# Optimization experiments

Hardware: AMD Instinct MI355X
Metric: run time of the kernel (lower is better)

Reference implementation:

```python
import jax, jax.numpy as jnp
import numpy as np

EPS = 1e-6

def rms_norm(x):
    # x / sqrt(mean(x^2, axis=-1) + eps)
    return x * jax.lax.rsqrt(jnp.mean(x * x, axis=-1, keepdims=True) + EPS)

def setup_inputs() -> dict:
    key = jax.random.key(0)
    k1, k2, k3 = jax.random.split(key, 3)
    T, B, D = 2048, 16, 1024
    x = jax.random.normal(k1, (T, B, D), dtype=jnp.float32)
    h0 = jax.random.normal(k2, (B, D), dtype=jnp.float32)
    # Orthogonal-ish init scaled by 0.5 (faithful to nn.init.orthogonal_ then *0.5)
    A = jax.random.normal(k3, (D, D), dtype=jnp.float32)
    Q, _ = jnp.linalg.qr(A)
    W = 0.5 * Q
    b = jnp.zeros((D,), dtype=jnp.float32)
    log_alpha = jnp.asarray(np.log(0.1), dtype=jnp.float32)
    return {"x": x, "h0": h0, "W": W, "b": b, "log_alpha": log_alpha}

def reference(x, h0, W, b, log_alpha):
    T, B, D = x.shape
    alpha = jnp.exp(log_alpha)
    # Precompute Wx for all timesteps: [T, B, D]
    Wx_all = jnp.einsum('tbd,ed->tbe', x, W) + b

    def step(h_prev, wx_t):
        h_raw = h_prev + alpha * wx_t
        h_new = rms_norm(h_raw)
        out = h_new * jax.nn.silu(h_new)
        return h_new, (h_new, out)

    _, (h_seq, output) = jax.lax.scan(step, h0, Wx_all)
    h = jnp.concatenate([h0[None], h_seq], axis=0)  # [T+1, B, D]
    return output, h
```

## Files before the change

### kernel.cpp

```cpp
#include <hip/hip_runtime.h>
#include <hip/hip_bf16.h>

#define TT 2048
#define BB 16
#define DD 1024
#define BD (BB*DD)
#define MR (TT*BB)
#define EPSV 1e-6f
#define INVD (1.0f/1024.0f)
#define CH 256
#define NCH (TT/CH)
#define RING 8

typedef __bf16 bf16x8_t __attribute__((ext_vector_type(8)));
typedef float  f32x4_t  __attribute__((ext_vector_type(4)));
typedef float  f32x2    __attribute__((ext_vector_type(2)));
typedef __attribute__((address_space(1))) void gvoid_t;
typedef __attribute__((address_space(3))) void lvoid_t;
typedef __attribute__((address_space(3))) float2 lds_f2;

union F4 { f32x4_t q; float4 v; f32x2 h[2]; float f[4]; };

static __device__ __forceinline__ f32x2 pk_mul(f32x2 a, f32x2 b) {
    f32x2 d; asm("v_pk_mul_f32 %0, %1, %2" : "=v"(d) : "v"(a), "v"(b)); return d;
}
static __device__ __forceinline__ f32x2 pk_fma(f32x2 a, f32x2 b, f32x2 c) {
    f32x2 d; asm("v_pk_fma_f32 %0, %1, %2, %3" : "=v"(d) : "v"(a), "v"(b), "v"(c)); return d;
}
static __device__ __forceinline__ f32x2 pk_add(f32x2 a, f32x2 b) {
    f32x2 d; asm("v_pk_add_f32 %0, %1, %2" : "=v"(d) : "v"(a), "v"(b)); return d;
}
static __device__ __forceinline__ float wave_red_sum(float ss) {
    asm volatile(
        "s_nop 1\n\t"
        "v_add_f32 %0, %0, %0 row_shr:1 bound_ctrl:0\n\t"
        "s_nop 1\n\t"
        "v_add_f32 %0, %0, %0 row_shr:2 bound_ctrl:0\n\t"
        "s_nop 1\n\t"
        "v_add_f32 %0, %0, %0 row_shr:4 bank_mask:0xe\n\t"
        "s_nop 1\n\t"
        "v_add_f32 %0, %0, %0 row_shr:8 bank_mask:0xc\n\t"
        "s_nop 1\n\t"
        "v_add_f32 %0, %0, %0 row_bcast:15 row_mask:0xa\n\t"
        "s_nop 1\n\t"
        "v_add_f32 %0, %0, %0 row_bcast:31 row_mask:0xc\n\t"
        "s_nop 1"
        : "+v"(ss));
    return __builtin_bit_cast(float, __builtin_amdgcn_readlane(__builtin_bit_cast(int, ss), 63));
}

static __device__ __forceinline__ unsigned short f2bf(float f) {
    __hip_bfloat16 h = __float2bfloat16(f);
    return __builtin_bit_cast(unsigned short, h);
}

__global__ void k_convert(const float* __restrict__ x, const float* __restrict__ W,
                          unsigned short* __restrict__ xb, unsigned short* __restrict__ wb) {
    const long NX4 = (long)MR * DD / 4;
    const long NW4 = (long)DD * DD / 4;
    const long stride = (long)gridDim.x * blockDim.x;
    for (long j = (long)blockIdx.x * blockDim.x + threadIdx.x; j < NX4 + NW4; j += stride) {
        const float4* src; unsigned short* dst; long o;
        if (j < NX4) { src = (const float4*)x; dst = xb; o = j; }
        else         { src = (const float4*)W; dst = wb; o = j - NX4; }
        float4 v = src[o];
        ushort4 u;
        u.x = f2bf(v.x); u.y = f2bf(v.y); u.z = f2bf(v.z); u.w = f2bf(v.w);
        *(ushort4*)(dst + o * 4) = u;
    }
}

__global__ __launch_bounds__(256, 2)
void k_gemm(const unsigned short* __restrict__ A, const unsigned short* __restrict__ Bw,
            const float* __restrict__ bias, float* __restrict__ C) {
    __shared__ char lds[16384];
    char* ldsA = lds;
    char* ldsB = lds + 8192;
    const int tid  = threadIdx.x;
    const int lane = tid & 63;
    const int wid  = tid >> 6;
    const int wm = wid >> 1, wn = wid & 1;
    const size_t arow0 = (size_t)blockIdx.y * 128;
    const int    brow0 = blockIdx.x * 128;

    f32x4_t acc[4][4] = {};

    const int off0 = tid * 16,        row0_ = off0 >> 6, colb0 = off0 & 63;
    const int off1 = 4096 + tid * 16, row1_ = off1 >> 6, colb1 = off1 & 63;

    for (int kk = 0; kk < DD / 32; ++kk) {
        const int kbase = kk * 32;
        __builtin_amdgcn_global_load_lds(
            (gvoid_t*)(A + (arow0 + row0_) * DD + kbase + (colb0 >> 1)),
            (lvoid_t*)(ldsA + off0), 16, 0, 0);
        __builtin_amdgcn_global_load_lds(
            (gvoid_t*)(A + (arow0 + row1_) * DD + kbase + (colb1 >> 1)),
            (lvoid_t*)(ldsA + off1), 16, 0, 0);
        __builtin_amdgcn_global_load_lds(
            (gvoid_t*)(Bw + (size_t)(brow0 + row0_) * DD + kbase + (colb0 >> 1)),
            (lvoid_t*)(ldsB + off0), 16, 0, 0);
        __builtin_amdgcn_global_load_lds(
            (gvoid_t*)(Bw + (size_t)(brow0 + row1_) * DD + kbase + (colb1 >> 1)),
            (lvoid_t*)(ldsB + off1), 16, 0, 0);
        __syncthreads();

        const int ml = lane & 15;
        const int kh = (lane >> 4) * 16;
        bf16x8_t av[4], bv[4];
        #pragma unroll
        for (int i = 0; i < 4; ++i) {
            av[i] = *(const bf16x8_t*)(ldsA + (wm * 64 + i * 16 + ml) * 64 + kh);
            bv[i] = *(const bf16x8_t*)(ldsB + (wn * 64 + i * 16 + ml) * 64 + kh);
        }
        #pragma unroll
        for (int i = 0; i < 4; ++i)
            #pragma unroll
            for (int j = 0; j < 4; ++j)
                acc[i][j] = __builtin_amdgcn_mfma_f32_16x16x32_bf16(av[i], bv[j], acc[i][j], 0, 0, 0);
        __syncthreads();
    }

    const int rq = (lane >> 4) * 4;
    const int cl = lane & 15;
    #pragma unroll
    for (int i = 0; i < 4; ++i) {
        #pragma unroll
        for (int j = 0; j < 4; ++j) {
            const int n = brow0 + wn * 64 + j * 16 + cl;
            const float bb = bias[n];
            #pragma unroll
            for (int q = 0; q < 4; ++q) {
                const size_t m = arow0 + wm * 64 + i * 16 + rq + q;
                C[m * DD + n] = acc[i][j][q] + bb;
            }
        }
    }
}

__global__ __launch_bounds__(256)
void k_gq(const float* __restrict__ Wx, const float* __restrict__ la,
          float2* __restrict__ gq_g) {
    const int b = blockIdx.y;
    const int wid = threadIdx.x >> 6, lane = threadIdx.x & 63;
    const int j0 = blockIdx.x * 16 + wid * 4;
    const float alpha = expf(la[0]);
    const float a2 = alpha * alpha;
    const int dof = lane * 4;
    const float* base = Wx + b * DD + dof;

    F4 R[5][4];
    #pragma unroll
    for (int jj = 0; jj < 5; ++jj) {
        const int row = max(j0 - 1 + jj, 0);
        #pragma unroll
        for (int k = 0; k < 4; ++k)
            R[jj][k].v = *(const float4*)(base + (size_t)row * BD + k * 256);
    }
    float red[8];
    #pragma unroll
    for (int sI = 0; sI < 4; ++sI) {
        float g = 0.f, q = 0.f;
        #pragma unroll
        for (int k = 0; k < 4; ++k)
            #pragma unroll
            for (int j = 0; j < 4; ++j) {
                const float w0 = R[sI][k].f[j], w1 = R[sI + 1][k].f[j];
                g = fmaf(w0, w1, g);
                q = fmaf(w1, w1, q);
            }
        red[sI] = g; red[4 + sI] = q;
    }
    #pragma unroll
    for (int m = 1; m < 64; m <<= 1)
        #pragma unroll
        for (int k = 0; k < 8; ++k)
            red[k] += __shfl_xor(red[k], m, 64);
    if (lane == 0) {
        #pragma unroll
        for (int sI = 0; sI < 4; ++sI) {
            const int j = j0 + sI;
            gq_g[(size_t)b * TT + j] =
                make_float2(j == 0 ? 0.f : a2 * red[sI], a2 * red[4 + sI]);
        }
    }
}

__global__ __launch_bounds__(64, 1)
void k_phaseA(const float* __restrict__ Wx, const float* __restrict__ h0,
              const float* __restrict__ la, const float2* __restrict__ gq_g,
              float* __restrict__ hout, float* __restrict__ rtab) {
    __shared__ float2 gqlds[TT];
    const int b = blockIdx.x;
    const int lane = threadIdx.x;
    const int dof = lane * 4;
    const float alpha = expf(la[0]);
    const float* wbase = Wx + b * DD + dof;

    {
        const float4* src = (const float4*)(gq_g + (size_t)b * TT);
        float4* dst = (float4*)gqlds;
        #pragma unroll
        for (int i = 0; i < 16; ++i) dst[i * 64 + lane] = src[i * 64 + lane];
    }
    f32x2 hraw[8];
    #pragma unroll
    for (int k = 0; k < 4; ++k) {
        F4 u; u.v = *(const float4*)(h0 + b * DD + k * 256 + dof);
        hraw[2*k] = u.h[0]; hraw[2*k+1] = u.h[1];
        *(float4*)(hout + b * DD + k * 256 + dof) = u.v;
    }
    asm volatile("" :: "v"(hraw[0]), "v"(hraw[1]), "v"(hraw[2]), "v"(hraw[3]),
                       "v"(hraw[4]), "v"(hraw[5]), "v"(hraw[6]), "v"(hraw[7]));
    asm volatile("s_waitcnt lgkmcnt(0)" ::: "memory");
    __builtin_amdgcn_sched_barrier(0);

    F4 buf[RING][4];
    #pragma unroll
    for (int s = 0; s < RING; ++s) {
        const float* wp = wbase + (size_t)s * BD;
        #pragma unroll
        for (int k = 0; k < 4; ++k)
            asm volatile("global_load_dwordx4 %0, %1, off"
                         : "=v"(buf[s][k].q) : "v"(wp + k * 256));
    }
    asm volatile("s_waitcnt vmcnt(24)" ::: "memory");
    __builtin_amdgcn_sched_barrier(0);

    float ss, ee[2], vr1 = 1.f, vr2 = 1.f;
    {
        f32x2 sa = pk_mul(hraw[0], hraw[0]);
        #pragma unroll
        for (int p = 1; p < 8; ++p) sa = pk_fma(hraw[p], hraw[p], sa);
        ss = wave_red_sum(sa[0] + sa[1]);
        f32x2 da = pk_mul(hraw[0], buf[0][0].h[0]);
        f32x2 ea = pk_mul(hraw[0], buf[1][0].h[0]);
        #pragma unroll
        for (int p = 1; p < 8; ++p) {
            da = pk_fma(hraw[p], buf[0][p>>1].h[p&1], da);
            ea = pk_fma(hraw[p], buf[1][p>>1].h[p&1], ea);
        }
        ee[1] = alpha * wave_red_sum(da[0] + da[1]);
        ee[0] = alpha * wave_red_sum(ea[0] + ea[1]);
    }
    f32x2 g2v[2];
    asm volatile("ds_read_b64 %0, %1" : "=v"(g2v[1]) : "v"((lds_f2*)&gqlds[0]));
    asm volatile("ds_read_b64 %0, %1" : "=v"(g2v[0]) : "v"((lds_f2*)&gqlds[1]));
    asm volatile("s_waitcnt lgkmcnt(0)" ::: "memory");
    __builtin_amdgcn_sched_barrier(0);

    float r_keep = 0.f;

    for (int tt = 0; tt < TT; tt += RING) {
        #pragma unroll
        for (int s = 0; s < RING; ++s) {
            const int m = tt + s;
            const int pe = (s + 1) & 1;

            if (s == 0 && (tt & 255) == 0) {
                float* hp = hout + (size_t)tt * BD + b * DD;
                const f32x2 rr0 = {vr1, vr1};
                #pragma unroll
                for (int k = 0; k < 4; ++k) {
                    F4 u;
                    u.h[0] = pk_mul(rr0, hraw[2*k]);
                    u.h[1] = pk_mul(rr0, hraw[2*k+1]);
                    *(float4*)(hp + k * 256 + dof) = u.v;
                }
            }

            asm volatile("s_waitcnt vmcnt(20)" ::: "memory");
            __builtin_amdgcn_sched_barrier(0);
            asm volatile("s_waitcnt lgkmcnt(1)" ::: "memory");
            __builtin_amdgcn_sched_barrier(0);

            const float Dp = fmaf(vr2, ee[pe], g2v[pe][0]);
            const float u1 = fmaf(vr1, ss, Dp + Dp);
            ss = fmaf(vr1, u1, g2v[pe][1]);
            const float rt = __builtin_amdgcn_rsqf(fmaf(ss, INVD, EPSV));
            r_keep = (lane == (m & 63)) ? rt : r_keep;

            const f32x2 rr1 = {vr1, vr1};
            const f32x2 aav = {alpha, alpha};
            #pragma unroll
            for (int k = 0; k < 4; ++k) {
                hraw[2*k]   = pk_fma(rr1, hraw[2*k],   pk_mul(aav, buf[s][k].h[0]));
                hraw[2*k+1] = pk_fma(rr1, hraw[2*k+1], pk_mul(aav, buf[s][k].h[1]));
            }

            {
                const F4* B = buf[(s + 2) & (RING - 1)];
                f32x2 ea0 = pk_mul(hraw[0], B[0].h[0]);
                f32x2 ea1 = pk_mul(hraw[1], B[0].h[1]);
                f32x2 ea2 = pk_mul(hraw[2], B[1].h[0]);
                f32x2 ea3 = pk_mul(hraw[3], B[1].h[1]);
                ea0 = pk_fma(hraw[4], B[2].h[0], ea0);
                ea1 = pk_fma(hraw[5], B[2].h[1], ea1);
                ea2 = pk_fma(hraw[6], B[3].h[0], ea2);
                ea3 = pk_fma(hraw[7], B[3].h[1], ea3);
                ea0 = pk_add(ea0, ea1); ea2 = pk_add(ea2, ea3); ea0 = pk_add(ea0, ea2);
                ee[pe] = alpha * wave_red_sum(ea0[0] + ea0[1]);
            }

            asm volatile("ds_read_b64 %0, %1"
                         : "=v"(g2v[pe]) : "v"((lds_f2*)&gqlds[(m + 2) & (TT - 1)]));

            {
                const float* wp = wbase + (size_t)((m + RING) & (TT - 1)) * BD;
                #pragma unroll
                for (int k = 0; k < 4; ++k)
                    asm volatile("global_load_dwordx4 %0, %1, off"
                                 : "=v"(buf[s][k].q) : "v"(wp + k * 256));
            }

            vr2 = vr1; vr1 = rt;
        }

        if ((tt & 63) == 56)
            rtab[(size_t)b * TT + (tt - 56) + lane] = r_keep;
    }

    asm volatile("s_waitcnt vmcnt(0) lgkmcnt(0)" ::: "memory");
}

__global__ __launch_bounds__(256)
void k_phaseB(float* __restrict__ WxOut, float* __restrict__ hout,
              const float* __restrict__ rtab, const float* __restrict__ la) {
    const int col = blockIdx.x * 256 + threadIdx.x;
    const int c = blockIdx.y;
    const int b = col >> 10;
    const float alpha = expf(la[0]);
    const float* rr = rtab + b * TT;
    float h = hout[(size_t)(c * CH) * BD + col];
    const int t0 = c * CH + 1;
    float w = WxOut[(size_t)(t0 - 1) * BD + col];
    for (int s = 0; s < CH; ++s) {
        const int t = t0 + s;
        float wnext = 0.f;
        if (s + 1 < CH) wnext = WxOut[(size_t)t * BD + col];
        const float r = rr[t - 1];
        const float hraw = fmaf(alpha, w, h);
        const float hn = r * hraw;
        const float sg = 1.0f / (1.0f + __expf(-hn));
        WxOut[(size_t)(t - 1) * BD + col] = hn * hn * sg;
        if ((t & (CH - 1)) != 0 || t == TT)
            hout[(size_t)t * BD + col] = hn;
        h = hn;
        w = wnext;
    }
}

extern "C" void kernel_launch(void* const* d_in, const int* in_sizes, int n_in,
                              void* d_out, int out_size, void* d_ws, size_t ws_size,
                              hipStream_t stream) {
    (void)in_sizes; (void)n_in; (void)out_size; (void)ws_size;
    const float* x    = (const float*)d_in[0];
    const float* h0   = (const float*)d_in[1];
    const float* W    = (const float*)d_in[2];
    const float* bias = (const float*)d_in[3];
    const float* la   = (const float*)d_in[4];

    float* outr = (float*)d_out;
    float* hreg = outr + (size_t)TT * BD;
    unsigned short* xb = (unsigned short*)hreg;
    unsigned short* wb = xb + (size_t)MR * DD;
    float2* gq_g = (float2*)(hreg + BD);
    float*  rtab = (float*)d_ws;

    k_convert<<<2048, 256, 0, stream>>>(x, W, xb, wb);
    k_gemm<<<dim3(DD / 128, MR / 128), 256, 0, stream>>>(xb, wb, bias, outr);
    k_gq<<<dim3(TT / 16, BB), 256, 0, stream>>>(outr, la, gq_g);
    k_phaseA<<<BB, 64, 0, stream>>>(outr, h0, la, gq_g, hreg, rtab);
    k_phaseB<<<dim3(BD / 256, NCH), 256, 0, stream>>>(outr, hreg, rtab, la);
}
```

Measured before the change: 542.5 us.

## Stage Wx rows through an LDS ring filled by dedicated producer waves

The sequential recurrence kernel now launches 5 waves per batch row. Four producer waves stream Wx rows into a 32-row LDS ring via global_load_lds, and the single compute wave reads rows from LDS with ds_read_b128 instead of issuing its own global loads. The aim is to take global-memory latency off the serial critical path by prefetching deeper. The cost is a block-wide barrier every 8 timesteps, 128KB of LDS per block, and LDS read latency on each step in place of the register ring.

Measured after the change: 547.7 us. About the same (+1.0%).

```diff
diff --git a/kernel.cpp b/kernel.cpp
--- a/kernel.cpp
+++ b/kernel.cpp
@@ -10,13 +10,13 @@
 #define INVD (1.0f/1024.0f)
 #define CH 256
 #define NCH (TT/CH)
-#define RING 8
 
 typedef __bf16 bf16x8_t __attribute__((ext_vector_type(8)));
 typedef float  f32x4_t  __attribute__((ext_vector_type(4)));
 typedef float  f32x2    __attribute__((ext_vector_type(2)));
 typedef __attribute__((address_space(1))) void gvoid_t;
 typedef __attribute__((address_space(3))) void lvoid_t;
+typedef __attribute__((address_space(3))) float  lds_f;
 typedef __attribute__((address_space(3))) float2 lds_f2;
 
 union F4 { f32x4_t q; float4 v; f32x2 h[2]; float f[4]; };
@@ -185,22 +185,61 @@
     }
 }
 
-__global__ __launch_bounds__(64, 1)
+__global__ __launch_bounds__(320, 1)
 void k_phaseA(const float* __restrict__ Wx, const float* __restrict__ h0,
               const float* __restrict__ la, const float2* __restrict__ gq_g,
               float* __restrict__ hout, float* __restrict__ rtab) {
+    __shared__ float  ring[32 * DD];
     __shared__ float2 gqlds[TT];
     const int b = blockIdx.x;
-    const int lane = threadIdx.x;
+    const int tid = threadIdx.x;
+    const int wid = tid >> 6;
+    const int lane = tid & 63;
+    const float alpha = expf(la[0]);
+
+    if (wid > 0) {
+        const int l = wid - 1;
+        const float* src = Wx + b * DD + lane * 4;
+        #pragma unroll
+        for (int q = 0; q < 3; ++q)
+            #pragma unroll
+            for (int j = 0; j < 2; ++j) {
+                const int row = q * 8 + l * 2 + j;
+                #pragma unroll
+                for (int k = 0; k < 4; ++k)
+                    __builtin_amdgcn_global_load_lds(
+                        (gvoid_t*)(src + (size_t)row * BD + k * 256),
+                        (lvoid_t*)(ring + (row & 31) * DD + k * 256), 16, 0, 0);
+            }
+        asm volatile("s_waitcnt vmcnt(8)" ::: "memory");
+        __builtin_amdgcn_s_barrier();
+        for (int p = 0; p < 256; ++p) {
+            if (p <= 252) {
+                const int q = p + 3;
+                #pragma unroll
+                for (int j = 0; j < 2; ++j) {
+                    const int row = q * 8 + l * 2 + j;
+                    #pragma unroll
+                    for (int k = 0; k < 4; ++k)
+                        __builtin_amdgcn_global_load_lds(
+                            (gvoid_t*)(src + (size_t)row * BD + k * 256),
+                            (lvoid_t*)(ring + (row & 31) * DD + k * 256), 16, 0, 0);
+                }
+                asm volatile("s_waitcnt vmcnt(8)" ::: "memory");
+            } else {
+                asm volatile("s_waitcnt vmcnt(0)" ::: "memory");
+            }
+            __builtin_amdgcn_s_barrier();
+        }
+        return;
+    }
+
     const int dof = lane * 4;
-    const float alpha = expf(la[0]);
-    const float* wbase = Wx + b * DD + dof;
-
     {
-        const float4* src = (const float4*)(gq_g + (size_t)b * TT);
+        const float4* src4 = (const float4*)(gq_g + (size_t)b * TT);
         float4* dst = (float4*)gqlds;
         #pragma unroll
-        for (int i = 0; i < 16; ++i) dst[i * 64 + lane] = src[i * 64 + lane];
+        for (int i = 0; i < 16; ++i) dst[i * 64 + lane] = src4[i * 64 + lane];
     }
     f32x2 hraw[8];
     #pragma unroll
@@ -213,51 +252,48 @@
                        "v"(hraw[4]), "v"(hraw[5]), "v"(hraw[6]), "v"(hraw[7]));
     asm volatile("s_waitcnt lgkmcnt(0)" ::: "memory");
     __builtin_amdgcn_sched_barrier(0);
-
-    F4 buf[RING][4];
-    #pragma unroll
-    for (int s = 0; s < RING; ++s) {
-        const float* wp = wbase + (size_t)s * BD;
+    __builtin_amdgcn_s_barrier();
+
+    F4 wReg[4][4];
+    #pragma unroll
+    for (int j = 0; j < 4; ++j)
         #pragma unroll
         for (int k = 0; k < 4; ++k)
-            asm volatile("global_load_dwordx4 %0, %1, off"
-                         : "=v"(buf[s][k].q) : "v"(wp + k * 256));
-    }
-    asm volatile("s_waitcnt vmcnt(24)" ::: "memory");
-    __builtin_amdgcn_sched_barrier(0);
-
-    float ss, ee[2], vr1 = 1.f, vr2 = 1.f;
-    {
-        f32x2 sa = pk_mul(hraw[0], hraw[0]);
-        #pragma unroll
-        for (int p = 1; p < 8; ++p) sa = pk_fma(hraw[p], hraw[p], sa);
-        ss = wave_red_sum(sa[0] + sa[1]);
-        f32x2 da = pk_mul(hraw[0], buf[0][0].h[0]);
-        f32x2 ea = pk_mul(hraw[0], buf[1][0].h[0]);
-        #pragma unroll
-        for (int p = 1; p < 8; ++p) {
-            da = pk_fma(hraw[p], buf[0][p>>1].h[p&1], da);
-            ea = pk_fma(hraw[p], buf[1][p>>1].h[p&1], ea);
-        }
-        ee[1] = alpha * wave_red_sum(da[0] + da[1]);
-        ee[0] = alpha * wave_red_sum(ea[0] + ea[1]);
-    }
+            asm volatile("ds_read_b128 %0, %1"
+                         : "=v"(wReg[j][k].q)
+                         : "v"((lds_f*)(ring + j * DD + k * 256 + dof)));
     f32x2 g2v[2];
     asm volatile("ds_read_b64 %0, %1" : "=v"(g2v[1]) : "v"((lds_f2*)&gqlds[0]));
     asm volatile("ds_read_b64 %0, %1" : "=v"(g2v[0]) : "v"((lds_f2*)&gqlds[1]));
     asm volatile("s_waitcnt lgkmcnt(0)" ::: "memory");
     __builtin_amdgcn_sched_barrier(0);
 
+    float ss, ee[2], vr1 = 1.f, vr2 = 1.f;
+    {
+        f32x2 sa = pk_mul(hraw[0], hraw[0]);
+        #pragma unroll
+        for (int p = 1; p < 8; ++p) sa = pk_fma(hraw[p], hraw[p], sa);
+        ss = wave_red_sum(sa[0] + sa[1]);
+        f32x2 da = pk_mul(hraw[0], wReg[0][0].h[0]);
+        f32x2 ea = pk_mul(hraw[0], wReg[1][0].h[0]);
+        #pragma unroll
+        for (int p = 1; p < 8; ++p) {
+            da = pk_fma(hraw[p], wReg[0][p>>1].h[p&1], da);
+            ea = pk_fma(hraw[p], wReg[1][p>>1].h[p&1], ea);
+        }
+        ee[1] = alpha * wave_red_sum(da[0] + da[1]);
+        ee[0] = alpha * wave_red_sum(ea[0] + ea[1]);
+    }
     float r_keep = 0.f;
 
-    for (int tt = 0; tt < TT; tt += RING) {
-        #pragma unroll
-        for (int s = 0; s < RING; ++s) {
-            const int m = tt + s;
+    for (int p = 0; p < 256; ++p) {
+        #pragma unroll
+        for (int s = 0; s < 8; ++s) {
+            const int m = p * 8 + s;
             const int pe = (s + 1) & 1;
 
-            if (s == 0 && (tt & 255) == 0) {
-                float* hp = hout + (size_t)tt * BD + b * DD;
+            if (s == 0 && (p & 31) == 0) {
+                float* hp = hout + (size_t)m * BD + b * DD;
                 const f32x2 rr0 = {vr1, vr1};
                 #pragma unroll
                 for (int k = 0; k < 4; ++k) {
@@ -268,9 +304,7 @@
                 }
             }
 
-            asm volatile("s_waitcnt vmcnt(20)" ::: "memory");
-            __builtin_amdgcn_sched_barrier(0);
-            asm volatile("s_waitcnt lgkmcnt(1)" ::: "memory");
+            asm volatile("s_waitcnt lgkmcnt(5)" ::: "memory");
             __builtin_amdgcn_sched_barrier(0);
 
             const float Dp = fmaf(vr2, ee[pe], g2v[pe][0]);
@@ -283,12 +317,12 @@
             const f32x2 aav = {alpha, alpha};
             #pragma unroll
             for (int k = 0; k < 4; ++k) {
-                hraw[2*k]   = pk_fma(rr1, hraw[2*k],   pk_mul(aav, buf[s][k].h[0]));
-                hraw[2*k+1] = pk_fma(rr1, hraw[2*k+1], pk_mul(aav, buf[s][k].h[1]));
+                hraw[2*k]   = pk_fma(rr1, hraw[2*k],   pk_mul(aav, wReg[s & 3][k].h[0]));
+                hraw[2*k+1] = pk_fma(rr1, hraw[2*k+1], pk_mul(aav, wReg[s & 3][k].h[1]));
             }
 
             {
-                const F4* B = buf[(s + 2) & (RING - 1)];
+                const F4* B = wReg[(s + 2) & 3];
                 f32x2 ea0 = pk_mul(hraw[0], B[0].h[0]);
                 f32x2 ea1 = pk_mul(hraw[1], B[0].h[1]);
                 f32x2 ea2 = pk_mul(hraw[2], B[1].h[0]);
@@ -305,18 +339,28 @@
                          : "=v"(g2v[pe]) : "v"((lds_f2*)&gqlds[(m + 2) & (TT - 1)]));
 
             {
-                const float* wp = wbase + (size_t)((m + RING) & (TT - 1)) * BD;
-                #pragma unroll
-                for (int k = 0; k < 4; ++k)
-                    asm volatile("global_load_dwordx4 %0, %1, off"
-                                 : "=v"(buf[s][k].q) : "v"(wp + k * 256));
+                const int slot = (m + 4) & 31;
+                asm volatile("ds_read_b128 %0, %1"
+                             : "=v"(wReg[s & 3][0].q)
+                             : "v"((lds_f*)(ring + slot * DD + 0 * 256 + dof)));
+                asm volatile("ds_read_b128 %0, %1"
+                             : "=v"(wReg[s & 3][1].q)
+                             : "v"((lds_f*)(ring + slot * DD + 1 * 256 + dof)));
+                asm volatile("ds_read_b128 %0, %1"
+                             : "=v"(wReg[s & 3][2].q)
+                             : "v"((lds_f*)(ring + slot * DD + 2 * 256 + dof)));
+                asm volatile("ds_read_b128 %0, %1"
+                             : "=v"(wReg[s & 3][3].q)
+                             : "v"((lds_f*)(ring + slot * DD + 3 * 256 + dof)));
             }
 
             vr2 = vr1; vr1 = rt;
         }
 
-        if ((tt & 63) == 56)
-            rtab[(size_t)b * TT + (tt - 56) + lane] = r_keep;
+        if ((p & 7) == 7)
+            rtab[(size_t)b * TT + (p - 7) * 8 + lane] = r_keep;
+
+        __builtin_amdgcn_s_barrier();
     }
 
     asm volatile("s_waitcnt vmcnt(0) lgkmcnt(0)" ::: "memory");
@@ -369,6 +413,6 @@
     k_convert<<<2048, 256, 0, stream>>>(x, W, xb, wb);
     k_gemm<<<dim3(DD / 128, MR / 128), 256, 0, stream>>>(xb, wb, bias, outr);
     k_gq<<<dim3(TT / 16, BB), 256, 0, stream>>>(outr, la, gq_g);
-    k_phaseA<<<BB, 64, 0, stream>>>(outr, h0, la, gq_g, hreg, rtab);
+    k_phaseA<<<BB, 320, 0, stream>>>(outr, h0, la, gq_g, hreg, rtab);
     k_phaseB<<<dim3(BD / 256, NCH), 256, 0, stream>>>(outr, hreg, rtab, la);
 }
```

## Stream bf16 batch-contiguous Wx copy into serial recurrence kernel

Applied to the files above, without the earlier changes.

k_gq now also writes a bf16 copy of Wx laid out batch-major and contiguous per batch. The serial phaseA kernel streams from this copy, so each step fetches half the bytes with contiguous per-lane loads. The recurrence state is rescaled by 1/alpha to remove one multiply per element per step. Chunk-head h values are stashed in scratch rows, and phaseB is split into two passes so it can write every h row without clobbering those heads. In exchange the dot products use bf16-rounded Wx, which lowers accuracy, and there is an extra write pass plus one more kernel launch.

Result: slower. 600.7 us (+10.7%).

```diff
diff --git a/kernel.cpp b/kernel.cpp
--- a/kernel.cpp
+++ b/kernel.cpp
@@ -15,6 +15,7 @@
 typedef __bf16 bf16x8_t __attribute__((ext_vector_type(8)));
 typedef float  f32x4_t  __attribute__((ext_vector_type(4)));
 typedef float  f32x2    __attribute__((ext_vector_type(2)));
+typedef unsigned int u32x4 __attribute__((ext_vector_type(4)));
 typedef __attribute__((address_space(1))) void gvoid_t;
 typedef __attribute__((address_space(3))) void lvoid_t;
 typedef __attribute__((address_space(3))) float2 lds_f2;
@@ -52,6 +53,16 @@
 static __device__ __forceinline__ unsigned short f2bf(float f) {
     __hip_bfloat16 h = __float2bfloat16(f);
     return __builtin_bit_cast(unsigned short, h);
+}
+
+static __device__ __forceinline__ void unpack_row(const u32x4* r, f32x2* w) {
+    #pragma unroll
+    for (int i = 0; i < 4; ++i) {
+        w[i][0]     = __builtin_bit_cast(float, r[0][i] << 16);
+        w[i][1]     = __builtin_bit_cast(float, r[0][i] & 0xFFFF0000u);
+        w[4 + i][0] = __builtin_bit_cast(float, r[1][i] << 16);
+        w[4 + i][1] = __builtin_bit_cast(float, r[1][i] & 0xFFFF0000u);
+    }
 }
 
 __global__ void k_convert(const float* __restrict__ x, const float* __restrict__ W,
@@ -139,7 +150,7 @@
 
 __global__ __launch_bounds__(256)
 void k_gq(const float* __restrict__ Wx, const float* __restrict__ la,
-          float2* __restrict__ gq_g) {
+          float2* __restrict__ gq_g, unsigned short* __restrict__ wxb) {
     const int b = blockIdx.y;
     const int wid = threadIdx.x >> 6, lane = threadIdx.x & 63;
     const int j0 = blockIdx.x * 16 + wid * 4;
@@ -156,6 +167,19 @@
         for (int k = 0; k < 4; ++k)
             R[jj][k].v = *(const float4*)(base + (size_t)row * BD + k * 256);
     }
+    {
+        unsigned short* wdst = wxb + ((size_t)b * TT + j0) * DD + dof;
+        #pragma unroll
+        for (int sI = 0; sI < 4; ++sI) {
+            #pragma unroll
+            for (int k = 0; k < 4; ++k) {
+                float4 v = R[sI + 1][k].v;
+                ushort4 u;
+                u.x = f2bf(v.x); u.y = f2bf(v.y); u.z = f2bf(v.z); u.w = f2bf(v.w);
+                *(ushort4*)(wdst + (size_t)sI * DD + k * 256) = u;
+            }
+        }
+    }
     float red[8];
     #pragma unroll
     for (int sI = 0; sI < 4; ++sI) {
@@ -186,15 +210,16 @@
 }
 
 __global__ __launch_bounds__(64, 1)
-void k_phaseA(const float* __restrict__ Wx, const float* __restrict__ h0,
+void k_phaseA(const unsigned short* __restrict__ Wxb, const float* __restrict__ h0,
               const float* __restrict__ la, const float2* __restrict__ gq_g,
-              float* __restrict__ hout, float* __restrict__ rtab) {
+              float* __restrict__ hreg, float* __restrict__ rtab) {
     __shared__ float2 gqlds[TT];
     const int b = blockIdx.x;
     const int lane = threadIdx.x;
-    const int dof = lane * 4;
+    const int eoff = lane * 16;
     const float alpha = expf(la[0]);
-    const float* wbase = Wx + b * DD + dof;
+    const float a2 = alpha * alpha;
+    const unsigned short* wbase = Wxb + (size_t)b * TT * DD + eoff;
 
     {
         const float4* src = (const float4*)(gq_g + (size_t)b * TT);
@@ -202,45 +227,51 @@
         #pragma unroll
         for (int i = 0; i < 16; ++i) dst[i * 64 + lane] = src[i * 64 + lane];
     }
-    f32x2 hraw[8];
-    #pragma unroll
-    for (int k = 0; k < 4; ++k) {
-        F4 u; u.v = *(const float4*)(h0 + b * DD + k * 256 + dof);
-        hraw[2*k] = u.h[0]; hraw[2*k+1] = u.h[1];
-        *(float4*)(hout + b * DD + k * 256 + dof) = u.v;
-    }
-    asm volatile("" :: "v"(hraw[0]), "v"(hraw[1]), "v"(hraw[2]), "v"(hraw[3]),
-                       "v"(hraw[4]), "v"(hraw[5]), "v"(hraw[6]), "v"(hraw[7]));
+    f32x2 q[8];
+    {
+        const float inva = 1.0f / alpha;
+        #pragma unroll
+        for (int k = 0; k < 4; ++k) {
+            float4 v = *(const float4*)(h0 + b * DD + eoff + k * 4);
+            *(float4*)(hreg + b * DD + eoff + k * 4) = v;
+            q[2*k][0]   = v.x * inva; q[2*k][1]   = v.y * inva;
+            q[2*k+1][0] = v.z * inva; q[2*k+1][1] = v.w * inva;
+        }
+    }
+    asm volatile("" :: "v"(q[0]), "v"(q[1]), "v"(q[2]), "v"(q[3]),
+                       "v"(q[4]), "v"(q[5]), "v"(q[6]), "v"(q[7]));
     asm volatile("s_waitcnt lgkmcnt(0)" ::: "memory");
     __builtin_amdgcn_sched_barrier(0);
 
-    F4 buf[RING][4];
+    u32x4 ring[RING][2];
     #pragma unroll
     for (int s = 0; s < RING; ++s) {
-        const float* wp = wbase + (size_t)s * BD;
-        #pragma unroll
-        for (int k = 0; k < 4; ++k)
-            asm volatile("global_load_dwordx4 %0, %1, off"
-                         : "=v"(buf[s][k].q) : "v"(wp + k * 256));
-    }
-    asm volatile("s_waitcnt vmcnt(24)" ::: "memory");
+        const unsigned short* wp = wbase + (size_t)s * DD;
+        asm volatile("global_load_dwordx4 %0, %1, off" : "=v"(ring[s][0]) : "v"(wp));
+        asm volatile("global_load_dwordx4 %0, %1, off" : "=v"(ring[s][1]) : "v"(wp + 8));
+    }
+    asm volatile("s_waitcnt vmcnt(12)" ::: "memory");
     __builtin_amdgcn_sched_barrier(0);
+
+    f32x2 wf[4][8];
+    unpack_row(ring[0], wf[0]);
+    unpack_row(ring[1], wf[1]);
 
     float ss, ee[2], vr1 = 1.f, vr2 = 1.f;
     {
-        f32x2 sa = pk_mul(hraw[0], hraw[0]);
-        #pragma unroll
-        for (int p = 1; p < 8; ++p) sa = pk_fma(hraw[p], hraw[p], sa);
-        ss = wave_red_sum(sa[0] + sa[1]);
-        f32x2 da = pk_mul(hraw[0], buf[0][0].h[0]);
-        f32x2 ea = pk_mul(hraw[0], buf[1][0].h[0]);
+        f32x2 sa = pk_mul(q[0], q[0]);
+        #pragma unroll
+        for (int p = 1; p < 8; ++p) sa = pk_fma(q[p], q[p], sa);
+        ss = a2 * wave_red_sum(sa[0] + sa[1]);
+        f32x2 da = pk_mul(q[0], wf[0][0]);
+        f32x2 ea = pk_mul(q[0], wf[1][0]);
         #pragma unroll
         for (int p = 1; p < 8; ++p) {
-            da = pk_fma(hraw[p], buf[0][p>>1].h[p&1], da);
-            ea = pk_fma(hraw[p], buf[1][p>>1].h[p&1], ea);
-        }
-        ee[1] = alpha * wave_red_sum(da[0] + da[1]);
-        ee[0] = alpha * wave_red_sum(ea[0] + ea[1]);
+            da = pk_fma(q[p], wf[0][p], da);
+            ea = pk_fma(q[p], wf[1][p], ea);
+        }
+        ee[1] = a2 * wave_red_sum(da[0] + da[1]);
+        ee[0] = a2 * wave_red_sum(ea[0] + ea[1]);
     }
     f32x2 g2v[2];
     asm volatile("ds_read_b64 %0, %1" : "=v"(g2v[1]) : "v"((lds_f2*)&gqlds[0]));
@@ -256,20 +287,22 @@
             const int m = tt + s;
             const int pe = (s + 1) & 1;
 
-            if (s == 0 && (tt & 255) == 0) {
-                float* hp = hout + (size_t)tt * BD + b * DD;
-                const f32x2 rr0 = {vr1, vr1};
+            if (s == 0 && tt >= 512 && (tt & 511) == 0) {
+                float* hp = hreg + (size_t)(256 + (tt >> 9)) * BD + b * DD + eoff;
+                const float svr = vr1 * alpha;
                 #pragma unroll
                 for (int k = 0; k < 4; ++k) {
-                    F4 u;
-                    u.h[0] = pk_mul(rr0, hraw[2*k]);
-                    u.h[1] = pk_mul(rr0, hraw[2*k+1]);
-                    *(float4*)(hp + k * 256 + dof) = u.v;
+                    float4 v;
+                    v.x = q[2*k][0] * svr;   v.y = q[2*k][1] * svr;
+                    v.z = q[2*k+1][0] * svr; v.w = q[2*k+1][1] * svr;
+                    *(float4*)(hp + k * 4) = v;
                 }
             }
 
-            asm volatile("s_waitcnt vmcnt(20)" ::: "memory");
+            asm volatile("s_waitcnt vmcnt(10)" ::: "memory");
             __builtin_amdgcn_sched_barrier(0);
+            unpack_row(ring[(s + 2) & (RING - 1)], wf[(s + 2) & 3]);
+
             asm volatile("s_waitcnt lgkmcnt(1)" ::: "memory");
             __builtin_amdgcn_sched_barrier(0);
 
@@ -280,36 +313,31 @@
             r_keep = (lane == (m & 63)) ? rt : r_keep;
 
             const f32x2 rr1 = {vr1, vr1};
-            const f32x2 aav = {alpha, alpha};
             #pragma unroll
-            for (int k = 0; k < 4; ++k) {
-                hraw[2*k]   = pk_fma(rr1, hraw[2*k],   pk_mul(aav, buf[s][k].h[0]));
-                hraw[2*k+1] = pk_fma(rr1, hraw[2*k+1], pk_mul(aav, buf[s][k].h[1]));
-            }
+            for (int p = 0; p < 8; ++p)
+                q[p] = pk_fma(rr1, q[p], wf[s & 3][p]);
 
             {
-                const F4* B = buf[(s + 2) & (RING - 1)];
-                f32x2 ea0 = pk_mul(hraw[0], B[0].h[0]);
-                f32x2 ea1 = pk_mul(hraw[1], B[0].h[1]);
-                f32x2 ea2 = pk_mul(hraw[2], B[1].h[0]);
-                f32x2 ea3 = pk_mul(hraw[3], B[1].h[1]);
-                ea0 = pk_fma(hraw[4], B[2].h[0], ea0);
-                ea1 = pk_fma(hraw[5], B[2].h[1], ea1);
-                ea2 = pk_fma(hraw[6], B[3].h[0], ea2);
-                ea3 = pk_fma(hraw[7], B[3].h[1], ea3);
+                const f32x2* B = wf[(s + 2) & 3];
+                f32x2 ea0 = pk_mul(q[0], B[0]);
+                f32x2 ea1 = pk_mul(q[1], B[1]);
+                f32x2 ea2 = pk_mul(q[2], B[2]);
+                f32x2 ea3 = pk_mul(q[3], B[3]);
+                ea0 = pk_fma(q[4], B[4], ea0);
+                ea1 = pk_fma(q[5], B[5], ea1);
+                ea2 = pk_fma(q[6], B[6], ea2);
+                ea3 = pk_fma(q[7], B[7], ea3);
                 ea0 = pk_add(ea0, ea1); ea2 = pk_add(ea2, ea3); ea0 = pk_add(ea0, ea2);
-                ee[pe] = alpha * wave_red_sum(ea0[0] + ea0[1]);
+                ee[pe] = a2 * wave_red_sum(ea0[0] + ea0[1]);
             }
 
             asm volatile("ds_read_b64 %0, %1"
                          : "=v"(g2v[pe]) : "v"((lds_f2*)&gqlds[(m + 2) & (TT - 1)]));
 
             {
-                const float* wp = wbase + (size_t)((m + RING) & (TT - 1)) * BD;
-                #pragma unroll
-                for (int k = 0; k < 4; ++k)
-                    asm volatile("global_load_dwordx4 %0, %1, off"
-                                 : "=v"(buf[s][k].q) : "v"(wp + k * 256));
+                const unsigned short* wp = wbase + (size_t)((m + RING) & (TT - 1)) * DD;
+                asm volatile("global_load_dwordx4 %0, %1, off" : "=v"(ring[s][0]) : "v"(wp));
+                asm volatile("global_load_dwordx4 %0, %1, off" : "=v"(ring[s][1]) : "v"(wp + 8));
             }
 
             vr2 = vr1; vr1 = rt;
@@ -324,13 +352,14 @@
 
 __global__ __launch_bounds__(256)
 void k_phaseB(float* __restrict__ WxOut, float* __restrict__ hout,
-              const float* __restrict__ rtab, const float* __restrict__ la) {
+              const float* __restrict__ rtab, const float* __restrict__ la, int pass) {
     const int col = blockIdx.x * 256 + threadIdx.x;
-    const int c = blockIdx.y;
+    const int c = blockIdx.y * 2 + pass;
     const int b = col >> 10;
     const float alpha = expf(la[0]);
     const float* rr = rtab + b * TT;
-    float h = hout[(size_t)(c * CH) * BD + col];
+    const int headrow = (c == 0) ? 0 : ((c & 1) ? c * CH : 256 + (c >> 1));
+    float h = hout[(size_t)headrow * BD + col];
     const int t0 = c * CH + 1;
     float w = WxOut[(size_t)(t0 - 1) * BD + col];
     for (int s = 0; s < CH; ++s) {
@@ -342,8 +371,7 @@
         const float hn = r * hraw;
         const float sg = 1.0f / (1.0f + __expf(-hn));
         WxOut[(size_t)(t - 1) * BD + col] = hn * hn * sg;
-        if ((t & (CH - 1)) != 0 || t == TT)
-            hout[(size_t)t * BD + col] = hn;
+        hout[(size_t)t * BD + col] = hn;
         h = hn;
         w = wnext;
     }
@@ -361,14 +389,16 @@
 
     float* outr = (float*)d_out;
     float* hreg = outr + (size_t)TT * BD;
-    unsigned short* xb = (unsigned short*)hreg;
-    unsigned short* wb = xb + (size_t)MR * DD;
-    float2* gq_g = (float2*)(hreg + BD);
-    float*  rtab = (float*)d_ws;
+    unsigned short* xb  = (unsigned short*)hreg;
+    unsigned short* wb  = (unsigned short*)(hreg + (size_t)1024 * BD);
+    float2*         gq_g = (float2*)(hreg + BD);
+    unsigned short* wxb = (unsigned short*)(hreg + (size_t)1025 * BD);
+    float*          rtab = (float*)d_ws;
 
     k_convert<<<2048, 256, 0, stream>>>(x, W, xb, wb);
     k_gemm<<<dim3(DD / 128, MR / 128), 256, 0, stream>>>(xb, wb, bias, outr);
-    k_gq<<<dim3(TT / 16, BB), 256, 0, stream>>>(outr, la, gq_g);
-    k_phaseA<<<BB, 64, 0, stream>>>(outr, h0, la, gq_g, hreg, rtab);
-    k_phaseB<<<dim3(BD / 256, NCH), 256, 0, stream>>>(outr, hreg, rtab, la);
-}
+    k_gq<<<dim3(TT / 16, BB), 256, 0, stream>>>(outr, la, gq_g, wxb);
+    k_phaseA<<<BB, 64, 0, stream>>>(wxb, h0, la, gq_g, hreg, rtab);
+    k_phaseB<<<dim3(BD / 256, NCH / 2), 256, 0, stream>>>(outr, hreg, rtab, la, 0);
+    k_phaseB<<<dim3(BD / 256, NCH / 2), 256, 0, stream>>>(outr, hreg, rtab, la, 1);
+}
```
